# Optimization experiments

Hardware: AMD Instinct MI355X
Metric: run time of the kernel (lower is better)

The kernel has to match this reference:

```python
import jax, jax.numpy as jnp
import numpy as np

B, H, L = 8, 256, 8192

def setup_inputs() -> dict:
    key = jax.random.key(0)
    k1, k2, k3 = jax.random.split(key, 3)
    u = jax.random.normal(k1, (B, H, L), dtype=jnp.float32)
    K = jax.random.normal(k2, (H, L), dtype=jnp.float32)
    # D ~ uniform_ring with min=max=1.0, field='real' -> random signs on unit ring
    D = jnp.where(jax.random.uniform(k3, (H,)) < 0.5, -1.0, 1.0).astype(jnp.float32)
    return {"u": u, "K": K, "D": D}

def reference(u, K, D):
    # FFT-based circular long convolution per channel: y = ifft(fft(u) * fft(K)).real
    u_s = jnp.fft.fft(u, axis=-1)            # (B,H,L) complex
    k_s = jnp.fft.fft(K, axis=-1)            # (H,L)   complex
    y = jnp.fft.ifft(u_s * k_s[None], axis=-1).real  # (B,H,L)
    y = y + D[None, :, None] * u             # skip connection D*u
    y = jnp.tanh(y)
    return y
```

## Files before the change

kernel.cpp:

```cpp
#include <hip/hip_runtime.h>
#include <math.h>


#define LL 8192
#define NT 512
#define HH 256
#define TWO_PI 6.2831853071795864f
#define CP8  0.92387953251129f
#define SP8  0.38268343236509f
#define CP4  0.70710678118654752f
#define SP4  0.70710678118654752f

__device__ __forceinline__ int SW(int e) {
    return e ^ ((e >> 3) & 0x18) ^ ((e >> 5) & 0x0E);
}
__device__ __forceinline__ int SW2(int e) {
    return e ^ (((e >> 5) & 7) << 2);
}
__device__ __forceinline__ float fast_tanh(float x) {
    float e = __expf(2.0f * x);
    return 1.0f - 2.0f / (e + 1.0f);
}

template<int JT>
__device__ __forceinline__ void fill_pyr_cs(float c0, float s0, float Er, float Ei,
                                            float* twr, float* twi) {
    const int off = (1 << JT) - 1;
    twr[off] = c0; twi[off] = s0;
    #pragma unroll
    for (int m = 1; m < (1 << JT); ++m) {
        const float pr = twr[off + m - 1], pi = twi[off + m - 1];
        twr[off + m] = pr * Er - pi * Ei;
        twi[off + m] = pr * Ei + pi * Er;
    }
    #pragma unroll
    for (int j = JT - 1; j >= 0; --j) {
        #pragma unroll
        for (int m = 0; m < (1 << j); ++m) {
            const float a = twr[(2 << j) - 1 + m], b = twi[(2 << j) - 1 + m];
            twr[(1 << j) - 1 + m] = a * a - b * b;
            twi[(1 << j) - 1 + m] = 2.0f * a * b;
        }
    }
}
template<int JT>
__device__ __forceinline__ void fill_pyr(float ang0, float Er, float Ei,
                                         float* twr, float* twi) {
    float s, c;
    __sincosf(ang0, &s, &c);
    fill_pyr_cs<JT>(c, s, Er, Ei, twr, twi);
}

template<int R2>
__device__ __forceinline__ void dif_apply(float* xr, float* xi,
                                          const float* twr, const float* twi) {
    #pragma unroll
    for (int j = R2 - 1; j >= 0; --j) {
        #pragma unroll
        for (int q = 0; q < (1 << (R2 - 1)); ++q) {
            const int mm = q & ((1 << j) - 1);
            const int m0 = ((q >> j) << (j + 1)) | mm;
            const int m1 = m0 + (1 << j);
            const float wr = twr[(1 << j) - 1 + mm], wi = twi[(1 << j) - 1 + mm];
            const float ar = xr[m0], ai = xi[m0], br = xr[m1], bi = xi[m1];
            xr[m0] = ar + br; xi[m0] = ai + bi;
            const float dr = ar - br, di = ai - bi;
            xr[m1] = dr * wr - di * wi;
            xi[m1] = dr * wi + di * wr;
        }
    }
}
template<int R2>
__device__ __forceinline__ void dit_apply(float* xr, float* xi,
                                          const float* twr, const float* twi) {
    #pragma unroll
    for (int j = 0; j < R2; ++j) {
        #pragma unroll
        for (int q = 0; q < (1 << (R2 - 1)); ++q) {
            const int mm = q & ((1 << j) - 1);
            const int m0 = ((q >> j) << (j + 1)) | mm;
            const int m1 = m0 + (1 << j);
            const float wr = twr[(1 << j) - 1 + mm], wi = twi[(1 << j) - 1 + mm];
            const float br = xr[m1] * wr - xi[m1] * wi;
            const float bi = xr[m1] * wi + xi[m1] * wr;
            const float ar = xr[m0], ai = xi[m0];
            xr[m0] = ar + br; xi[m0] = ai + bi;
            xr[m1] = ar - br; xi[m1] = ai - bi;
        }
    }
}


__device__ __forceinline__ void fwd_A(float* xr, float* xi, int tid,
                                      float* re, float* im) {
    float twr[15], twi[15];
    fill_pyr<3>(-(TWO_PI / 8192.0f) * (float)tid, CP8, -SP8, twr, twi);
    dif_apply<4>(xr, xi, twr, twi);
    #pragma unroll
    for (int m = 0; m < 16; ++m) {
        const int p = SW(tid + (m << 9));
        re[p] = xr[m]; im[p] = xi[m];
    }
}

template<bool INV>
__device__ __forceinline__ void mid_M1(float* re, float* im, int lane, int wv) {
    float twr[7], twi[7];
    const float sgn = INV ? 1.0f : -1.0f;
    fill_pyr<2>(sgn * (TWO_PI / 512.0f) * (float)lane, CP4, sgn * SP4, twr, twi);
    #pragma unroll
    for (int r = 0; r < 2; ++r) {
        const int base = (((wv << 1) | r) << 9) + lane;
        float ar[8], ai[8];
        #pragma unroll
        for (int j = 0; j < 8; ++j) {
            const int p = SW(base + (j << 6));
            ar[j] = re[p]; ai[j] = im[p];
        }
        if (INV) dit_apply<3>(ar, ai, twr, twi);
        else     dif_apply<3>(ar, ai, twr, twi);
        #pragma unroll
        for (int j = 0; j < 8; ++j) {
            const int p = SW(base + (j << 6));
            re[p] = ar[j]; im[p] = ai[j];
        }
    }
}

template<bool INV>
__device__ __forceinline__ void mid_M2(float* re, float* im, int lane, int wv) {
    float twr[7], twi[7];
    const float sgn = INV ? 1.0f : -1.0f;
    fill_pyr<2>(sgn * (TWO_PI / 64.0f) * (float)(lane & 7), CP4, sgn * SP4, twr, twi);
    const int sub = ((lane >> 3) << 6) + (lane & 7);
    #pragma unroll
    for (int r = 0; r < 2; ++r) {
        const int base = (((wv << 1) | r) << 9) + sub;
        float ar[8], ai[8];
        #pragma unroll
        for (int j = 0; j < 8; ++j) {
            const int p = SW(base + (j << 3));
            ar[j] = re[p]; ai[j] = im[p];
        }
        if (INV) dit_apply<3>(ar, ai, twr, twi);
        else     dif_apply<3>(ar, ai, twr, twi);
        #pragma unroll
        for (int j = 0; j < 8; ++j) {
            const int p = SW(base + (j << 3));
            re[p] = ar[j]; im[p] = ai[j];
        }
    }
}

__global__ __launch_bounds__(NT, 4) void conv_kernel(const float* __restrict__ u,
                                                     const float2* __restrict__ Kf,
                                                     float* __restrict__ out) {
    __shared__ float re[LL];
    __shared__ float im[LL];
    const int tid = threadIdx.x;
    const int h = blockIdx.x & (HH - 1);
    const int pr_ = blockIdx.x >> 8;
    const size_t off0 = ((size_t)(pr_ * 2) * HH + h) * LL;
    const size_t off1 = off0 + (size_t)HH * LL;
    const float* u0 = u + off0;
    const float* u1 = u + off1;

    float xr[16], xi[16];
    #pragma unroll
    for (int m = 0; m < 16; ++m) {
        xr[m] = u0[tid + (m << 9)];
        xi[m] = u1[tid + (m << 9)];
    }
    fwd_A(xr, xi, tid, re, im);
    __syncthreads();

    const int lane = tid & 63, wv = tid >> 6;
    const int c0 = (wv << 1);

    float kwr[2][8], kwi[2][8];
    #pragma unroll
    for (int r = 0; r < 2; ++r) {
        const int eb = ((c0 | r) << 9) + (lane << 3);
        const float4* kp = (const float4*)(Kf + (size_t)h * LL + eb);
        #pragma unroll
        for (int jj = 0; jj < 4; ++jj) {
            const float4 v = kp[jj];
            kwr[r][2 * jj] = v.x;     kwi[r][2 * jj] = v.y;
            kwr[r][2 * jj + 1] = v.z; kwi[r][2 * jj + 1] = v.w;
        }
    }

    mid_M1<false>(re, im, lane, wv);
    mid_M2<false>(re, im, lane, wv);

    {
        float twd_r[7], twd_i[7], twu_r[7], twu_i[7];
        fill_pyr_cs<2>(1.0f, 0.0f, CP4, -SP4, twd_r, twd_i);
        fill_pyr_cs<2>(1.0f, 0.0f, CP4, SP4, twu_r, twu_i);
        #pragma unroll
        for (int r = 0; r < 2; ++r) {
            const int eb = ((c0 | r) << 9) + (lane << 3);
            float yr[8], yi[8];
            #pragma unroll
            for (int j = 0; j < 8; ++j) {
                const int p = SW(eb + j);
                yr[j] = re[p]; yi[j] = im[p];
            }
            dif_apply<3>(yr, yi, twd_r, twd_i);
            #pragma unroll
            for (int j = 0; j < 8; ++j) {
                const float a = yr[j], b = yi[j];
                yr[j] = a * kwr[r][j] - b * kwi[r][j];
                yi[j] = a * kwi[r][j] + b * kwr[r][j];
            }
            dit_apply<3>(yr, yi, twu_r, twu_i);
            #pragma unroll
            for (int j = 0; j < 8; ++j) {
                const int p = SW(eb + j);
                re[p] = yr[j]; im[p] = yi[j];
            }
        }
    }

    mid_M2<true>(re, im, lane, wv);
    mid_M1<true>(re, im, lane, wv);
    __syncthreads();

    {
        float twr[15], twi[15];
        #pragma unroll
        for (int m = 0; m < 16; ++m) {
            const int p = SW(tid + (m << 9));
            xr[m] = re[p]; xi[m] = im[p];
        }
        fill_pyr<3>((TWO_PI / 8192.0f) * (float)tid, CP8, SP8, twr, twi);
        dit_apply<4>(xr, xi, twr, twi);
    }
    float* o0 = out + off0;
    float* o1 = out + off1;
    #pragma unroll
    for (int m = 0; m < 16; ++m) {
        const int n = tid + (m << 9);
        o0[n] = fast_tanh(xr[m]);
        o1[n] = fast_tanh(xi[m]);
    }
}

__global__ __launch_bounds__(256) void kfft1_kernel(const float* __restrict__ K,
                                                    float2* __restrict__ Kf) {
    const int b = blockIdx.x;
    const int h = b >> 3, seg = b & 7;
    const int m = (seg << 8) + threadIdx.x;
    const float* Kr = K + (size_t)h * LL;
    const float A = Kr[m];
    const float B = Kr[m + 2048];
    const float C = Kr[m + 4096];
    const float E = Kr[m + 6144];
    float sn, cs;
    __sincosf(-(TWO_PI / 8192.0f) * (float)m, &sn, &cs);
    const float c2 = cs * cs - sn * sn, s2 = 2.0f * cs * sn;
    const float c3 = cs * c2 - sn * s2, s3 = cs * s2 + sn * c2;
    const float p = A - C, q = B - E;
    const float sum = A + C + B + E;
    const float dif = A + C - B - E;
    float2* o = Kf + (size_t)h * LL;
    o[m]        = make_float2(sum, 0.0f);
    o[m + 2048] = make_float2(dif * c2, dif * s2);
    o[m + 4096] = make_float2(p * cs + q * sn, p * sn - q * cs);
    o[m + 6144] = make_float2(p * c3 - q * s3, p * s3 + q * c3);
}

__global__ __launch_bounds__(256) void kfft2_kernel(float2* __restrict__ Kf,
                                                    const float* __restrict__ D) {
    __shared__ float re[2048];
    __shared__ float im[2048];
    const int b = blockIdx.x;
    const int h = b >> 2, cq = b & 3;
    const int tid = threadIdx.x;
    float2* base = Kf + (size_t)h * LL + (cq << 11);

    float xr[8], xi[8];
    #pragma unroll
    for (int m = 0; m < 8; ++m) {
        const float2 v = base[tid + (m << 8)];
        xr[m] = v.x; xi[m] = v.y;
    }
    {
        float twr[7], twi[7];
        fill_pyr<2>(-(TWO_PI / 2048.0f) * (float)tid, CP4, -SP4, twr, twi);
        dif_apply<3>(xr, xi, twr, twi);
    }
    #pragma unroll
    for (int m = 0; m < 8; ++m) {
        const int p = SW2(tid + (m << 8));
        re[p] = xr[m]; im[p] = xi[m];
    }
    __syncthreads();

    {
        const int t_ = tid & 31, sub = tid >> 5;
        float twr[7], twi[7];
        fill_pyr<2>(-(TWO_PI / 256.0f) * (float)t_, CP4, -SP4, twr, twi);
        const int be = (sub << 8) + t_;
        float ar[8], ai[8];
        #pragma unroll
        for (int j = 0; j < 8; ++j) {
            const int p = SW2(be + (j << 5));
            ar[j] = re[p]; ai[j] = im[p];
        }
        dif_apply<3>(ar, ai, twr, twi);
        #pragma unroll
        for (int j = 0; j < 8; ++j) {
            const int p = SW2(be + (j << 5));
            re[p] = ar[j]; im[p] = ai[j];
        }
    }

    {
        const int blk = tid >> 2, r = tid & 3;
        float twr[7], twi[7];
        fill_pyr<2>(-(TWO_PI / 32.0f) * (float)r, CP4, -SP4, twr, twi);
        const int eb = (blk << 5) + r;
        float yr[8], yi[8];
        #pragma unroll
        for (int j = 0; j < 8; ++j) {
            const int p = SW2(eb + (j << 2));
            yr[j] = re[p]; yi[j] = im[p];
        }
        dif_apply<3>(yr, yi, twr, twi);
        const float s2 = (r < 2) ? 1.0f : -1.0f;
        #pragma unroll
        for (int j = 0; j < 8; ++j) {
            const float vr = __shfl_xor(yr[j], 2);
            const float vi = __shfl_xor(yi[j], 2);
            const float tr = fmaf(yr[j], s2, vr);
            const float ti = fmaf(yi[j], s2, vi);
            yr[j] = (r == 3) ? ti : tr;
            yi[j] = (r == 3) ? -tr : ti;
        }
        const float s1 = (r & 1) ? -1.0f : 1.0f;
        #pragma unroll
        for (int j = 0; j < 8; ++j) {
            const float vr = __shfl_xor(yr[j], 1);
            const float vi = __shfl_xor(yi[j], 1);
            yr[j] = fmaf(yr[j], s1, vr);
            yi[j] = fmaf(yi[j], s1, vi);
        }
        const float dh = D[h];
        const float invN = 1.0f / (float)LL;
        #pragma unroll
        for (int j = 0; j < 8; ++j) {
            base[eb + (j << 2)] = make_float2((yr[j] + dh) * invN, yi[j] * invN);
        }
    }
}

extern "C" void kernel_launch(void* const* d_in, const int* in_sizes, int n_in,
                              void* d_out, int out_size, void* d_ws, size_t ws_size,
                              hipStream_t stream) {
    const float* u = (const float*)d_in[0];
    const float* K = (const float*)d_in[1];
    const float* D = (const float*)d_in[2];
    float* out = (float*)d_out;
    float2* Kf = (float2*)d_ws;

    kfft1_kernel<<<dim3(8 * HH), dim3(256), 0, stream>>>(K, Kf);
    kfft2_kernel<<<dim3(4 * HH), dim3(256), 0, stream>>>(Kf, D);
    conv_kernel<<<dim3(4 * HH), dim3(NT), 0, stream>>>(u, Kf, out);
}
```

Before: 154.4 us.

## Restructure conv FFT mid stages to radix-16 with shuffles; fuse kernel FFT launches

The conv kernel's middle FFT stages go from two radix-8 passes per direction to one radix-16 pass, plus a fused radix-16 pass with a lane-pair shuffle step. This cuts LDS round trips, and a simpler swizzle replaces the old one. The two K-spectrum kernels merge into one, which drops a launch and the intermediate global write and read. It also lowers launch_bounds occupancy from 4 to 2 to make room for the larger register arrays, which may cost latency hiding.

After: 169.6 us. 9.8% more time.

```diff
diff --git a/kernel.cpp b/kernel.cpp
--- a/kernel.cpp
+++ b/kernel.cpp
@@ -6,13 +6,15 @@
 #define NT 512
 #define HH 256
 #define TWO_PI 6.2831853071795864f
+#define CP16 0.980785280403230f
+#define SP16 0.195090322016128f
 #define CP8  0.92387953251129f
 #define SP8  0.38268343236509f
 #define CP4  0.70710678118654752f
 #define SP4  0.70710678118654752f
 
-__device__ __forceinline__ int SW(int e) {
-    return e ^ ((e >> 3) & 0x18) ^ ((e >> 5) & 0x0E);
+__device__ __forceinline__ int SWc(int e) {
+    return e ^ ((e >> 5) & 0xF);
 }
 __device__ __forceinline__ int SW2(int e) {
     return e ^ (((e >> 5) & 7) << 2);
@@ -89,70 +91,28 @@
         }
     }
 }
-
-
-__device__ __forceinline__ void fwd_A(float* xr, float* xi, int tid,
-                                      float* re, float* im) {
-    float twr[15], twi[15];
-    fill_pyr<3>(-(TWO_PI / 8192.0f) * (float)tid, CP8, -SP8, twr, twi);
-    dif_apply<4>(xr, xi, twr, twi);
-    #pragma unroll
-    for (int m = 0; m < 16; ++m) {
-        const int p = SW(tid + (m << 9));
-        re[p] = xr[m]; im[p] = xi[m];
-    }
-}
-
-template<bool INV>
-__device__ __forceinline__ void mid_M1(float* re, float* im, int lane, int wv) {
-    float twr[7], twi[7];
-    const float sgn = INV ? 1.0f : -1.0f;
-    fill_pyr<2>(sgn * (TWO_PI / 512.0f) * (float)lane, CP4, sgn * SP4, twr, twi);
-    #pragma unroll
-    for (int r = 0; r < 2; ++r) {
-        const int base = (((wv << 1) | r) << 9) + lane;
-        float ar[8], ai[8];
-        #pragma unroll
-        for (int j = 0; j < 8; ++j) {
-            const int p = SW(base + (j << 6));
-            ar[j] = re[p]; ai[j] = im[p];
-        }
-        if (INV) dit_apply<3>(ar, ai, twr, twi);
-        else     dif_apply<3>(ar, ai, twr, twi);
-        #pragma unroll
-        for (int j = 0; j < 8; ++j) {
-            const int p = SW(base + (j << 6));
-            re[p] = ar[j]; im[p] = ai[j];
-        }
-    }
-}
-
-template<bool INV>
-__device__ __forceinline__ void mid_M2(float* re, float* im, int lane, int wv) {
-    float twr[7], twi[7];
-    const float sgn = INV ? 1.0f : -1.0f;
-    fill_pyr<2>(sgn * (TWO_PI / 64.0f) * (float)(lane & 7), CP4, sgn * SP4, twr, twi);
-    const int sub = ((lane >> 3) << 6) + (lane & 7);
-    #pragma unroll
-    for (int r = 0; r < 2; ++r) {
-        const int base = (((wv << 1) | r) << 9) + sub;
-        float ar[8], ai[8];
-        #pragma unroll
-        for (int j = 0; j < 8; ++j) {
-            const int p = SW(base + (j << 3));
-            ar[j] = re[p]; ai[j] = im[p];
-        }
-        if (INV) dit_apply<3>(ar, ai, twr, twi);
-        else     dif_apply<3>(ar, ai, twr, twi);
-        #pragma unroll
-        for (int j = 0; j < 8; ++j) {
-            const int p = SW(base + (j << 3));
-            re[p] = ar[j]; im[p] = ai[j];
-        }
-    }
-}
-
-__global__ __launch_bounds__(NT, 4) void conv_kernel(const float* __restrict__ u,
+template<int R2>
+__device__ __forceinline__ void dit_apply_c(float* xr, float* xi,
+                                            const float* twr, const float* twi) {
+    #pragma unroll
+    for (int j = 0; j < R2; ++j) {
+        #pragma unroll
+        for (int q = 0; q < (1 << (R2 - 1)); ++q) {
+            const int mm = q & ((1 << j) - 1);
+            const int m0 = ((q >> j) << (j + 1)) | mm;
+            const int m1 = m0 + (1 << j);
+            const float wr = twr[(1 << j) - 1 + mm], wi = -twi[(1 << j) - 1 + mm];
+            const float br = xr[m1] * wr - xi[m1] * wi;
+            const float bi = xr[m1] * wi + xi[m1] * wr;
+            const float ar = xr[m0], ai = xi[m0];
+            xr[m0] = ar + br; xi[m0] = ai + bi;
+            xr[m1] = ar - br; xi[m1] = ai - bi;
+        }
+    }
+}
+
+
+__global__ __launch_bounds__(NT, 2) void conv_kernel(const float* __restrict__ u,
                                                      const float2* __restrict__ Kf,
                                                      float* __restrict__ out) {
     __shared__ float re[LL];
@@ -171,66 +131,131 @@
         xr[m] = u0[tid + (m << 9)];
         xi[m] = u1[tid + (m << 9)];
     }
-    fwd_A(xr, xi, tid, re, im);
+    {
+        float twr[15], twi[15];
+        fill_pyr<3>(-(TWO_PI / 8192.0f) * (float)tid, CP8, -SP8, twr, twi);
+        dif_apply<4>(xr, xi, twr, twi);
+        #pragma unroll
+        for (int m = 0; m < 16; ++m) {
+            const int p = SWc(tid + (m << 9));
+            re[p] = xr[m]; im[p] = xi[m];
+        }
+    }
     __syncthreads();
 
     const int lane = tid & 63, wv = tid >> 6;
-    const int c0 = (wv << 1);
-
-    float kwr[2][8], kwi[2][8];
-    #pragma unroll
-    for (int r = 0; r < 2; ++r) {
-        const int eb = ((c0 | r) << 9) + (lane << 3);
-        const float4* kp = (const float4*)(Kf + (size_t)h * LL + eb);
-        #pragma unroll
-        for (int jj = 0; jj < 4; ++jj) {
+    const int t = lane & 31;
+    const int ch = (wv << 1) + (lane >> 5);
+    const int cb = ch << 9;
+    const int par = lane & 1;
+    const float s = par ? -1.0f : 1.0f;
+
+    float kwr[16], kwi[16];
+    {
+        const float4* kp = (const float4*)(Kf + (size_t)h * LL + cb + (t << 4));
+        #pragma unroll
+        for (int jj = 0; jj < 8; ++jj) {
             const float4 v = kp[jj];
-            kwr[r][2 * jj] = v.x;     kwi[r][2 * jj] = v.y;
-            kwr[r][2 * jj + 1] = v.z; kwi[r][2 * jj + 1] = v.w;
-        }
-    }
-
-    mid_M1<false>(re, im, lane, wv);
-    mid_M2<false>(re, im, lane, wv);
-
-    {
-        float twd_r[7], twd_i[7], twu_r[7], twu_i[7];
-        fill_pyr_cs<2>(1.0f, 0.0f, CP4, -SP4, twd_r, twd_i);
-        fill_pyr_cs<2>(1.0f, 0.0f, CP4, SP4, twu_r, twu_i);
-        #pragma unroll
-        for (int r = 0; r < 2; ++r) {
-            const int eb = ((c0 | r) << 9) + (lane << 3);
-            float yr[8], yi[8];
-            #pragma unroll
-            for (int j = 0; j < 8; ++j) {
-                const int p = SW(eb + j);
-                yr[j] = re[p]; yi[j] = im[p];
-            }
-            dif_apply<3>(yr, yi, twd_r, twd_i);
-            #pragma unroll
-            for (int j = 0; j < 8; ++j) {
-                const float a = yr[j], b = yi[j];
-                yr[j] = a * kwr[r][j] - b * kwi[r][j];
-                yi[j] = a * kwi[r][j] + b * kwr[r][j];
-            }
-            dit_apply<3>(yr, yi, twu_r, twu_i);
-            #pragma unroll
-            for (int j = 0; j < 8; ++j) {
-                const int p = SW(eb + j);
-                re[p] = yr[j]; im[p] = yi[j];
-            }
-        }
-    }
-
-    mid_M2<true>(re, im, lane, wv);
-    mid_M1<true>(re, im, lane, wv);
+            kwr[2 * jj]     = v.x; kwi[2 * jj]     = v.y;
+            kwr[2 * jj + 1] = v.z; kwi[2 * jj + 1] = v.w;
+        }
+    }
+
+    {
+        float twr[15], twi[15];
+        fill_pyr<3>(-(TWO_PI / 512.0f) * (float)t, CP8, -SP8, twr, twi);
+        const int base = cb + t;
+        float ar[16], ai[16];
+        #pragma unroll
+        for (int j = 0; j < 16; ++j) {
+            const int p = SWc(base + (j << 5));
+            ar[j] = re[p]; ai[j] = im[p];
+        }
+        dif_apply<4>(ar, ai, twr, twi);
+        #pragma unroll
+        for (int j = 0; j < 16; ++j) {
+            const int p = SWc(base + (j << 5));
+            re[p] = ar[j]; im[p] = ai[j];
+        }
+    }
+    {
+        float twd_r[15], twd_i[15];
+        fill_pyr_cs<3>(1.0f, 0.0f, CP8, -SP8, twd_r, twd_i);
+        const int base2 = cb + (t << 4);
+        float yr[16], yi[16];
+        #pragma unroll
+        for (int j = 0; j < 16; ++j) {
+            const int p = SWc(base2 + j);
+            yr[j] = re[p]; yi[j] = im[p];
+        }
+        #pragma unroll
+        for (int j = 0; j < 16; ++j) {
+            const float vr = __shfl_xor(yr[j], 1);
+            const float vi = __shfl_xor(yi[j], 1);
+            const float tr = fmaf(yr[j], s, vr);
+            const float ti = fmaf(yi[j], s, vi);
+            const float br = twd_r[7 + (j >> 1)], bi = twd_i[7 + (j >> 1)];
+            float wr_, wi_;
+            if (j & 1) { wr_ = CP16 * br + SP16 * bi; wi_ = CP16 * bi - SP16 * br; }
+            else       { wr_ = br;                    wi_ = bi; }
+            wr_ = par ? wr_ : 1.0f;
+            wi_ = par ? wi_ : 0.0f;
+            yr[j] = tr * wr_ - ti * wi_;
+            yi[j] = tr * wi_ + ti * wr_;
+        }
+        dif_apply<4>(yr, yi, twd_r, twd_i);
+        #pragma unroll
+        for (int j = 0; j < 16; ++j) {
+            const float a = yr[j], bb = yi[j];
+            yr[j] = a * kwr[j] - bb * kwi[j];
+            yi[j] = a * kwi[j] + bb * kwr[j];
+        }
+        dit_apply_c<4>(yr, yi, twd_r, twd_i);
+        #pragma unroll
+        for (int j = 0; j < 16; ++j) {
+            const float br = twd_r[7 + (j >> 1)], bi = twd_i[7 + (j >> 1)];
+            float wr_, wi_;
+            if (j & 1) { wr_ = CP16 * br + SP16 * bi; wi_ = CP16 * bi - SP16 * br; }
+            else       { wr_ = br;                    wi_ = bi; }
+            wr_ = par ? wr_ : 1.0f;
+            wi_ = par ? wi_ : 0.0f;
+            const float tr = yr[j] * wr_ + yi[j] * wi_;
+            const float ti = yi[j] * wr_ - yr[j] * wi_;
+            const float vr = __shfl_xor(tr, 1);
+            const float vi = __shfl_xor(ti, 1);
+            yr[j] = fmaf(tr, s, vr);
+            yi[j] = fmaf(ti, s, vi);
+        }
+        #pragma unroll
+        for (int j = 0; j < 16; ++j) {
+            const int p = SWc(base2 + j);
+            re[p] = yr[j]; im[p] = yi[j];
+        }
+    }
+    {
+        float twr[15], twi[15];
+        fill_pyr<3>((TWO_PI / 512.0f) * (float)t, CP8, SP8, twr, twi);
+        const int base = cb + t;
+        float ar[16], ai[16];
+        #pragma unroll
+        for (int j = 0; j < 16; ++j) {
+            const int p = SWc(base + (j << 5));
+            ar[j] = re[p]; ai[j] = im[p];
+        }
+        dit_apply<4>(ar, ai, twr, twi);
+        #pragma unroll
+        for (int j = 0; j < 16; ++j) {
+            const int p = SWc(base + (j << 5));
+            re[p] = ar[j]; im[p] = ai[j];
+        }
+    }
     __syncthreads();
 
     {
         float twr[15], twi[15];
         #pragma unroll
         for (int m = 0; m < 16; ++m) {
-            const int p = SW(tid + (m << 9));
+            const int p = SWc(tid + (m << 9));
             xr[m] = re[p]; xi[m] = im[p];
         }
         fill_pyr<3>((TWO_PI / 8192.0f) * (float)tid, CP8, SP8, twr, twi);
@@ -246,44 +271,44 @@
     }
 }
 
-__global__ __launch_bounds__(256) void kfft1_kernel(const float* __restrict__ K,
+__global__ __launch_bounds__(256) void kfftF_kernel(const float* __restrict__ K,
+                                                    const float* __restrict__ D,
                                                     float2* __restrict__ Kf) {
-    const int b = blockIdx.x;
-    const int h = b >> 3, seg = b & 7;
-    const int m = (seg << 8) + threadIdx.x;
-    const float* Kr = K + (size_t)h * LL;
-    const float A = Kr[m];
-    const float B = Kr[m + 2048];
-    const float C = Kr[m + 4096];
-    const float E = Kr[m + 6144];
-    float sn, cs;
-    __sincosf(-(TWO_PI / 8192.0f) * (float)m, &sn, &cs);
-    const float c2 = cs * cs - sn * sn, s2 = 2.0f * cs * sn;
-    const float c3 = cs * c2 - sn * s2, s3 = cs * s2 + sn * c2;
-    const float p = A - C, q = B - E;
-    const float sum = A + C + B + E;
-    const float dif = A + C - B - E;
-    float2* o = Kf + (size_t)h * LL;
-    o[m]        = make_float2(sum, 0.0f);
-    o[m + 2048] = make_float2(dif * c2, dif * s2);
-    o[m + 4096] = make_float2(p * cs + q * sn, p * sn - q * cs);
-    o[m + 6144] = make_float2(p * c3 - q * s3, p * s3 + q * c3);
-}
-
-__global__ __launch_bounds__(256) void kfft2_kernel(float2* __restrict__ Kf,
-                                                    const float* __restrict__ D) {
     __shared__ float re[2048];
     __shared__ float im[2048];
     const int b = blockIdx.x;
     const int h = b >> 2, cq = b & 3;
     const int tid = threadIdx.x;
-    float2* base = Kf + (size_t)h * LL + (cq << 11);
+    const float* Kr = K + (size_t)h * LL;
 
     float xr[8], xi[8];
     #pragma unroll
-    for (int m = 0; m < 8; ++m) {
-        const float2 v = base[tid + (m << 8)];
-        xr[m] = v.x; xi[m] = v.y;
+    for (int j = 0; j < 8; ++j) {
+        const int m = tid + (j << 8);
+        const float A  = Kr[m];
+        const float Bv = Kr[m + 2048];
+        const float C  = Kr[m + 4096];
+        const float E  = Kr[m + 6144];
+        if (cq == 0) {
+            xr[j] = A + C + Bv + E; xi[j] = 0.0f;
+        } else {
+            float sn, cs;
+            __sincosf(-(TWO_PI / 8192.0f) * (float)m, &sn, &cs);
+            if (cq == 1) {
+                const float dif = A + C - Bv - E;
+                const float c2 = cs * cs - sn * sn, s2 = 2.0f * cs * sn;
+                xr[j] = dif * c2; xi[j] = dif * s2;
+            } else {
+                const float p_ = A - C, q_ = Bv - E;
+                if (cq == 2) {
+                    xr[j] = p_ * cs + q_ * sn; xi[j] = p_ * sn - q_ * cs;
+                } else {
+                    const float c2 = cs * cs - sn * sn, s2 = 2.0f * cs * sn;
+                    const float c3 = cs * c2 - sn * s2, s3 = cs * s2 + sn * c2;
+                    xr[j] = p_ * c3 - q_ * s3; xi[j] = p_ * s3 + q_ * c3;
+                }
+            }
+        }
     }
     {
         float twr[7], twi[7];
@@ -291,12 +316,11 @@
         dif_apply<3>(xr, xi, twr, twi);
     }
     #pragma unroll
-    for (int m = 0; m < 8; ++m) {
-        const int p = SW2(tid + (m << 8));
-        re[p] = xr[m]; im[p] = xi[m];
+    for (int j = 0; j < 8; ++j) {
+        const int p = SW2(tid + (j << 8));
+        re[p] = xr[j]; im[p] = xi[j];
     }
     __syncthreads();
-
     {
         const int t_ = tid & 31, sub = tid >> 5;
         float twr[7], twi[7];
@@ -315,7 +339,6 @@
             re[p] = ar[j]; im[p] = ai[j];
         }
     }
-
     {
         const int blk = tid >> 2, r = tid & 3;
         float twr[7], twi[7];
@@ -328,29 +351,30 @@
             yr[j] = re[p]; yi[j] = im[p];
         }
         dif_apply<3>(yr, yi, twr, twi);
-        const float s2 = (r < 2) ? 1.0f : -1.0f;
+        const float s2_ = (r < 2) ? 1.0f : -1.0f;
         #pragma unroll
         for (int j = 0; j < 8; ++j) {
             const float vr = __shfl_xor(yr[j], 2);
             const float vi = __shfl_xor(yi[j], 2);
-            const float tr = fmaf(yr[j], s2, vr);
-            const float ti = fmaf(yi[j], s2, vi);
+            const float tr = fmaf(yr[j], s2_, vr);
+            const float ti = fmaf(yi[j], s2_, vi);
             yr[j] = (r == 3) ? ti : tr;
             yi[j] = (r == 3) ? -tr : ti;
         }
-        const float s1 = (r & 1) ? -1.0f : 1.0f;
+        const float s1_ = (r & 1) ? -1.0f : 1.0f;
         #pragma unroll
         for (int j = 0; j < 8; ++j) {
             const float vr = __shfl_xor(yr[j], 1);
             const float vi = __shfl_xor(yi[j], 1);
-            yr[j] = fmaf(yr[j], s1, vr);
-            yi[j] = fmaf(yi[j], s1, vi);
+            yr[j] = fmaf(yr[j], s1_, vr);
+            yi[j] = fmaf(yi[j], s1_, vi);
         }
         const float dh = D[h];
         const float invN = 1.0f / (float)LL;
-        #pragma unroll
-        for (int j = 0; j < 8; ++j) {
-            base[eb + (j << 2)] = make_float2((yr[j] + dh) * invN, yi[j] * invN);
+        float2* baseo = Kf + (size_t)h * LL + (cq << 11);
+        #pragma unroll
+        for (int j = 0; j < 8; ++j) {
+            baseo[eb + (j << 2)] = make_float2((yr[j] + dh) * invN, yi[j] * invN);
         }
     }
 }
@@ -364,7 +388,6 @@
     float* out = (float*)d_out;
     float2* Kf = (float2*)d_ws;
 
-    kfft1_kernel<<<dim3(8 * HH), dim3(256), 0, stream>>>(K, Kf);
-    kfft2_kernel<<<dim3(4 * HH), dim3(256), 0, stream>>>(Kf, D);
+    kfftF_kernel<<<dim3(4 * HH), dim3(256), 0, stream>>>(K, D, Kf);
     conv_kernel<<<dim3(4 * HH), dim3(NT), 0, stream>>>(u, Kf, out);
 }
```

## Fuse kernel-FFT first stage into second kernel and retune LDS swizzle

Applied to the files above, without the earlier changes.

Merges the radix-4 first pass over K into the per-quarter FFT kernel, so each block computes its quarter's twiddled inputs directly from K. This removes one launch and the write and re-read of the intermediate complex spectrum. In exchange, K is read four times, once per quarter block, and quarter branches diverge per block. The shared-memory swizzle used by the convolution kernel is also changed to a different XOR pattern to alter bank-conflict behaviour.

After: 148.8 us. 3.6% less time.

```diff
diff --git a/kernel.cpp b/kernel.cpp
--- a/kernel.cpp
+++ b/kernel.cpp
@@ -12,7 +12,7 @@
 #define SP4  0.70710678118654752f
 
 __device__ __forceinline__ int SW(int e) {
-    return e ^ ((e >> 3) & 0x18) ^ ((e >> 5) & 0x0E);
+    return e ^ ((e >> 4) & 0x18) ^ ((e >> 5) & 0x07);
 }
 __device__ __forceinline__ int SW2(int e) {
     return e ^ (((e >> 5) & 7) << 2);
@@ -246,44 +246,44 @@
     }
 }
 
-__global__ __launch_bounds__(256) void kfft1_kernel(const float* __restrict__ K,
+__global__ __launch_bounds__(256) void kfftF_kernel(const float* __restrict__ K,
+                                                    const float* __restrict__ D,
                                                     float2* __restrict__ Kf) {
-    const int b = blockIdx.x;
-    const int h = b >> 3, seg = b & 7;
-    const int m = (seg << 8) + threadIdx.x;
-    const float* Kr = K + (size_t)h * LL;
-    const float A = Kr[m];
-    const float B = Kr[m + 2048];
-    const float C = Kr[m + 4096];
-    const float E = Kr[m + 6144];
-    float sn, cs;
-    __sincosf(-(TWO_PI / 8192.0f) * (float)m, &sn, &cs);
-    const float c2 = cs * cs - sn * sn, s2 = 2.0f * cs * sn;
-    const float c3 = cs * c2 - sn * s2, s3 = cs * s2 + sn * c2;
-    const float p = A - C, q = B - E;
-    const float sum = A + C + B + E;
-    const float dif = A + C - B - E;
-    float2* o = Kf + (size_t)h * LL;
-    o[m]        = make_float2(sum, 0.0f);
-    o[m + 2048] = make_float2(dif * c2, dif * s2);
-    o[m + 4096] = make_float2(p * cs + q * sn, p * sn - q * cs);
-    o[m + 6144] = make_float2(p * c3 - q * s3, p * s3 + q * c3);
-}
-
-__global__ __launch_bounds__(256) void kfft2_kernel(float2* __restrict__ Kf,
-                                                    const float* __restrict__ D) {
     __shared__ float re[2048];
     __shared__ float im[2048];
     const int b = blockIdx.x;
     const int h = b >> 2, cq = b & 3;
     const int tid = threadIdx.x;
-    float2* base = Kf + (size_t)h * LL + (cq << 11);
+    const float* Kr = K + (size_t)h * LL;
 
     float xr[8], xi[8];
     #pragma unroll
-    for (int m = 0; m < 8; ++m) {
-        const float2 v = base[tid + (m << 8)];
-        xr[m] = v.x; xi[m] = v.y;
+    for (int j = 0; j < 8; ++j) {
+        const int m = tid + (j << 8);
+        const float A  = Kr[m];
+        const float Bv = Kr[m + 2048];
+        const float C  = Kr[m + 4096];
+        const float E  = Kr[m + 6144];
+        if (cq == 0) {
+            xr[j] = A + C + Bv + E; xi[j] = 0.0f;
+        } else {
+            float sn, cs;
+            __sincosf(-(TWO_PI / 8192.0f) * (float)m, &sn, &cs);
+            if (cq == 1) {
+                const float dif = A + C - Bv - E;
+                const float c2 = cs * cs - sn * sn, s2 = 2.0f * cs * sn;
+                xr[j] = dif * c2; xi[j] = dif * s2;
+            } else {
+                const float p_ = A - C, q_ = Bv - E;
+                if (cq == 2) {
+                    xr[j] = p_ * cs + q_ * sn; xi[j] = p_ * sn - q_ * cs;
+                } else {
+                    const float c2 = cs * cs - sn * sn, s2 = 2.0f * cs * sn;
+                    const float c3 = cs * c2 - sn * s2, s3 = cs * s2 + sn * c2;
+                    xr[j] = p_ * c3 - q_ * s3; xi[j] = p_ * s3 + q_ * c3;
+                }
+            }
+        }
     }
     {
         float twr[7], twi[7];
@@ -291,12 +291,11 @@
         dif_apply<3>(xr, xi, twr, twi);
     }
     #pragma unroll
-    for (int m = 0; m < 8; ++m) {
-        const int p = SW2(tid + (m << 8));
-        re[p] = xr[m]; im[p] = xi[m];
+    for (int j = 0; j < 8; ++j) {
+        const int p = SW2(tid + (j << 8));
+        re[p] = xr[j]; im[p] = xi[j];
     }
     __syncthreads();
-
     {
         const int t_ = tid & 31, sub = tid >> 5;
         float twr[7], twi[7];
@@ -315,7 +314,6 @@
             re[p] = ar[j]; im[p] = ai[j];
         }
     }
-
     {
         const int blk = tid >> 2, r = tid & 3;
         float twr[7], twi[7];
@@ -328,29 +326,30 @@
             yr[j] = re[p]; yi[j] = im[p];
         }
         dif_apply<3>(yr, yi, twr, twi);
-        const float s2 = (r < 2) ? 1.0f : -1.0f;
+        const float s2_ = (r < 2) ? 1.0f : -1.0f;
         #pragma unroll
         for (int j = 0; j < 8; ++j) {
             const float vr = __shfl_xor(yr[j], 2);
             const float vi = __shfl_xor(yi[j], 2);
-            const float tr = fmaf(yr[j], s2, vr);
-            const float ti = fmaf(yi[j], s2, vi);
+            const float tr = fmaf(yr[j], s2_, vr);
+            const float ti = fmaf(yi[j], s2_, vi);
             yr[j] = (r == 3) ? ti : tr;
             yi[j] = (r == 3) ? -tr : ti;
         }
-        const float s1 = (r & 1) ? -1.0f : 1.0f;
+        const float s1_ = (r & 1) ? -1.0f : 1.0f;
         #pragma unroll
         for (int j = 0; j < 8; ++j) {
             const float vr = __shfl_xor(yr[j], 1);
             const float vi = __shfl_xor(yi[j], 1);
-            yr[j] = fmaf(yr[j], s1, vr);
-            yi[j] = fmaf(yi[j], s1, vi);
+            yr[j] = fmaf(yr[j], s1_, vr);
+            yi[j] = fmaf(yi[j], s1_, vi);
         }
         const float dh = D[h];
         const float invN = 1.0f / (float)LL;
-        #pragma unroll
-        for (int j = 0; j < 8; ++j) {
-            base[eb + (j << 2)] = make_float2((yr[j] + dh) * invN, yi[j] * invN);
+        float2* baseo = Kf + (size_t)h * LL + (cq << 11);
+        #pragma unroll
+        for (int j = 0; j < 8; ++j) {
+            baseo[eb + (j << 2)] = make_float2((yr[j] + dh) * invN, yi[j] * invN);
         }
     }
 }
@@ -364,7 +363,6 @@
     float* out = (float*)d_out;
     float2* Kf = (float2*)d_ws;
 
-    kfft1_kernel<<<dim3(8 * HH), dim3(256), 0, stream>>>(K, Kf);
-    kfft2_kernel<<<dim3(4 * HH), dim3(256), 0, stream>>>(Kf, D);
+    kfftF_kernel<<<dim3(4 * HH), dim3(256), 0, stream>>>(K, D, Kf);
     conv_kernel<<<dim3(4 * HH), dim3(NT), 0, stream>>>(u, Kf, out);
 }
```
